# Kernel tuning notes

Hardware: AMD Instinct MI355X
Metric: run time of the kernel (lower is better)

The kernel has to match this reference:

```python
import jax, jax.numpy as jnp
import numpy as np

N = 4
IS_SLOW = (False, False, True, True)
RATES = (1, 1, 4, 4)
THRESH = 0.3
F2S_IDX = {(0, 2): 0, (0, 3): 1, (1, 2): 2, (1, 3): 3}


def _conv1d(x, w, stride, pad):
    # x: [B, C_in, T], w: [C_out, C_in, K]
    return jax.lax.conv_general_dilated(
        x, w, (stride,), [(pad, pad)], dimension_numbers=("NCH", "OIH", "NCH"))


def _linear_interp(x, t_out):
    # x: [B, D, T_in] -> [B, D, t_out]; matches F.interpolate(mode='linear', align_corners=False)
    t_in = x.shape[2]
    scale = t_in / t_out
    src = (jnp.arange(t_out, dtype=jnp.float32) + 0.5) * scale - 0.5
    src = jnp.clip(src, 0.0, float(t_in - 1))
    i0 = jnp.floor(src).astype(jnp.int32)
    i1 = jnp.minimum(i0 + 1, t_in - 1)
    w = (src - i0.astype(jnp.float32)).astype(x.dtype)
    return x[:, :, i0] * (1.0 - w) + x[:, :, i1] * w


def setup_inputs() -> dict:
    key = jax.random.key(0)
    ks = jax.random.split(key, 8)
    T_FAST, T_SLOW, B, D, H = 512, 128, 32, 1024, 256
    return {
        "feat0": jax.random.normal(ks[0], (T_FAST, B, D), jnp.float32),
        "feat1": jax.random.normal(ks[1], (T_FAST, B, D), jnp.float32),
        "feat2": jax.random.normal(ks[2], (T_SLOW, B, D), jnp.float32),
        "feat3": jax.random.normal(ks[3], (T_SLOW, B, D), jnp.float32),
        "mlp_w1": jax.random.normal(ks[4], (N * N, 2 * D, H), jnp.float32) * 0.02,
        "mlp_b1": jnp.zeros((N * N, H), jnp.float32),
        "mlp_w2": jax.random.normal(ks[5], (N * N, H, 1), jnp.float32) * 0.02,
        "mlp_b2": jnp.zeros((N * N, 1), jnp.float32),
        "s2f_w": jax.random.normal(ks[6], (D, D, 1), jnp.float32) * 0.02,
        "s2f_b": jnp.zeros((D,), jnp.float32),
        "f2s_w": jax.random.normal(ks[7], (4, D, D, 5), jnp.float32) * 0.02,
    }


def reference(feat0, feat1, feat2, feat3, mlp_w1, mlp_b1, mlp_w2, mlp_b2,
              s2f_w, s2f_b, f2s_w):
    feats = [feat0, feat1, feat2, feat3]            # [T_i, B, D]
    feats_bdt = [jnp.transpose(f, (1, 2, 0)) for f in feats]  # [B, D, T_i]
    globals_ = [f.mean(axis=2) for f in feats_bdt]  # [B, D]
    outputs = list(feats)
    for i in range(N):
        for j in range(N):
            if i == j:
                continue
            p = i * N + j
            pair_vec = jnp.concatenate([globals_[i], globals_[j]], axis=-1)  # [B, 2D]
            h = jax.nn.relu(pair_vec @ mlp_w1[p] + mlp_b1[p])
            score = jax.nn.sigmoid(h @ mlp_w2[p] + mlp_b2[p])[:, 0]          # [B]
            cond = score.mean() >= THRESH
            if IS_SLOW[i] and not IS_SLOW[j]:
                # slow -> fast: interpolate up, 1x1 conv proj, score-weighted residual
                up = _linear_interp(feats_bdt[i], feats_bdt[j].shape[2])
                up = _conv1d(up, s2f_w, 1, 0) + s2f_b[None, :, None]
                new = feats_bdt[j] + score[:, None, None] * up
                outputs[j] = jnp.where(cond, jnp.transpose(new, (2, 0, 1)), outputs[j])
            elif (not IS_SLOW[i]) and IS_SLOW[j]:
                # fast -> slow: strided conv down, score-weighted residual
                stride = RATES[j] // RATES[i]
                down = _conv1d(feats_bdt[i], f2s_w[F2S_IDX[(i, j)]], stride, 2)
                new = feats_bdt[j] + score[:, None, None] * down
                outputs[j] = jnp.where(cond, jnp.transpose(new, (2, 0, 1)), outputs[j])
    return tuple(outputs)
```

## Files before the change

kernel.cpp:

```cpp
#include <hip/hip_runtime.h>
#include <math.h>

typedef __bf16 bf16;
typedef bf16 bf16x8 __attribute__((ext_vector_type(8)));
typedef bf16 bf16x4 __attribute__((ext_vector_type(4)));
typedef float f32x4 __attribute__((ext_vector_type(4)));

#define OFF_GLOB   0ul
#define OFF_H      524288ul
#define OFF_SCORE  786432ul
#define OFF_COND   787456ul
#define OFF_PART   788480ul
#define OFF_PROJ   5242880ul
#define OFF_WTF2S  38797312ul
#define OFF_WTS2F  59768832ul


__device__ __forceinline__ void slot_ij(int s, int& i, int& j) {
  if (s < 4) { i = 2 + (s & 1); j = s >> 1; }
  else       { int ss = s - 4; i = ss & 1; j = 2 + (ss >> 1); }
}

__global__ __launch_bounds__(256) void k_means_part(
    const float* __restrict__ f0, const float* __restrict__ f1,
    const float* __restrict__ f2, const float* __restrict__ f3,
    float* __restrict__ part)
{
  int b = blockIdx.x, c = blockIdx.y, i = blockIdx.z, tid = threadIdx.x;
  const float* f = (i == 0) ? f0 : (i == 1) ? f1 : (i == 2) ? f2 : f3;
  int chunk = (i < 2) ? 64 : 16;
  int t0 = c * chunk;
  float4 s = make_float4(0.f, 0.f, 0.f, 0.f);
  for (int t = t0; t < t0 + chunk; ++t) {
    float4 v = ((const float4*)(f + (size_t)(t * 32 + b) * 1024))[tid];
    s.x += v.x; s.y += v.y; s.z += v.z; s.w += v.w;
  }
  ((float4*)part)[(size_t)((i * 8 + c) * 32 + b) * 256 + tid] = s;
}

__global__ __launch_bounds__(256) void k_means_final(
    const float* __restrict__ part, float* __restrict__ g)
{
  int b = blockIdx.x, i = blockIdx.y, tid = threadIdx.x;
  float4 s = make_float4(0.f, 0.f, 0.f, 0.f);
  for (int c = 0; c < 8; ++c) {
    float4 v = ((const float4*)part)[(size_t)((i * 8 + c) * 32 + b) * 256 + tid];
    s.x += v.x; s.y += v.y; s.z += v.z; s.w += v.w;
  }
  float inv = (i < 2) ? (1.f / 512.f) : (1.f / 128.f);
  s.x *= inv; s.y *= inv; s.z *= inv; s.w *= inv;
  ((float4*)g)[(size_t)(i * 32 + b) * 256 + tid] = s;
}

__global__ __launch_bounds__(256) void k_mlp1(
    const float* __restrict__ g, const float* __restrict__ w1, float* __restrict__ h_ws)
{
  int s = blockIdx.x, hc = blockIdx.y, kz = blockIdx.z, tid = threadIdx.x;
  int pi, pj; slot_ij(s, pi, pj);
  int p = pi * 4 + pj;
  int h = hc * 32 + (tid & 31);
  int bg = tid >> 5;
  __shared__ float pv[32 * 65];
  float acc0 = 0.f, acc1 = 0.f, acc2 = 0.f, acc3 = 0.f;
  for (int kt = 0; kt < 8; ++kt) {
    int k0 = kz * 512 + kt * 64;
    __syncthreads();
    for (int l = tid; l < 2048; l += 256) {
      int bb = l >> 6, kk = l & 63;
      int k = k0 + kk;
      float v = (k < 1024) ? g[(size_t)pi * 32768 + bb * 1024 + k]
                           : g[(size_t)pj * 32768 + bb * 1024 + (k - 1024)];
      pv[bb * 65 + kk] = v;
    }
    __syncthreads();
    const float* wp = w1 + ((size_t)p * 2048 + k0) * 256 + hc * 32 + (tid & 31);
    for (int kk = 0; kk < 64; ++kk) {
      float w = wp[(size_t)kk * 256];
      acc0 += pv[(bg * 4 + 0) * 65 + kk] * w;
      acc1 += pv[(bg * 4 + 1) * 65 + kk] * w;
      acc2 += pv[(bg * 4 + 2) * 65 + kk] * w;
      acc3 += pv[(bg * 4 + 3) * 65 + kk] * w;
    }
  }
  atomicAdd(&h_ws[(size_t)s * 8192 + (bg * 4 + 0) * 256 + h], acc0);
  atomicAdd(&h_ws[(size_t)s * 8192 + (bg * 4 + 1) * 256 + h], acc1);
  atomicAdd(&h_ws[(size_t)s * 8192 + (bg * 4 + 2) * 256 + h], acc2);
  atomicAdd(&h_ws[(size_t)s * 8192 + (bg * 4 + 3) * 256 + h], acc3);
}

__global__ __launch_bounds__(256) void k_mlp2(
    const float* __restrict__ h_ws, const float* __restrict__ b1,
    const float* __restrict__ w2, const float* __restrict__ b2,
    float* __restrict__ score, float* __restrict__ cond)
{
  int s = blockIdx.x, tid = threadIdx.x;
  int pi, pj; slot_ij(s, pi, pj);
  int p = pi * 4 + pj;
  float w2v = w2[p * 256 + tid];
  float b1v = b1[p * 256 + tid];
  float b2v = b2[p];
  __shared__ float red[4];
  float tot = 0.f;
  for (int b = 0; b < 32; ++b) {
    float v = fmaxf(h_ws[(size_t)s * 8192 + b * 256 + tid] + b1v, 0.f) * w2v;
    for (int off = 32; off > 0; off >>= 1) v += __shfl_down(v, off);
    if ((tid & 63) == 0) red[tid >> 6] = v;
    __syncthreads();
    if (tid == 0) {
      float sum = red[0] + red[1] + red[2] + red[3] + b2v;
      float sc = 1.f / (1.f + expf(-sum));
      score[s * 32 + b] = sc;
      tot += sc;
    }
    __syncthreads();
  }
  if (tid == 0) cond[s] = (tot * (1.f / 32.f) >= 0.3f) ? 1.f : 0.f;
}

__global__ __launch_bounds__(256) void k_f2s_transpose(
    const float* __restrict__ w, const float* __restrict__ cond, bf16* __restrict__ wT)
{
  int z = blockIdx.y, co = blockIdx.x, tid = threadIdx.x;
  int sel = (cond[5 + 2 * z] > 0.5f) ? 1 : ((cond[4 + 2 * z] > 0.5f) ? 0 : -1);
  if (sel < 0) return;
  int widx = sel * 2 + z;
  __shared__ float buf[5120];
  const float* src = w + ((size_t)widx * 1024 + co) * 5120;
  for (int l = tid; l < 5120; l += 256) buf[l] = src[l];
  __syncthreads();
  bf16* dst = wT + (size_t)z * 5242880 + (size_t)co * 5120;
  for (int o = tid; o < 5120; o += 256) {
    int kk = o >> 10, ci = o & 1023;
    dst[o] = (bf16)buf[ci * 5 + kk];
  }
}

__global__ __launch_bounds__(256) void k_s2f_convert(
    const float* __restrict__ w, bf16* __restrict__ wT)
{
  size_t gi = (size_t)blockIdx.x * 256 + threadIdx.x;
  float4 v = ((const float4*)w)[gi];
  bf16x4 o;
  o[0] = (bf16)v.x; o[1] = (bf16)v.y; o[2] = (bf16)v.z; o[3] = (bf16)v.w;
  *(bf16x4*)&wT[gi * 4] = o;
}

__global__ __launch_bounds__(256) void k_s2f_gemm(
    const float* __restrict__ feat2, const float* __restrict__ feat3,
    const bf16* __restrict__ wT, const float* __restrict__ s2f_b,
    const float* __restrict__ cond, float* __restrict__ proj)
{
  int z = blockIdx.z;
  int sel = (cond[1 + 2 * z] > 0.5f) ? 3 : ((cond[2 * z] > 0.5f) ? 2 : -1);
  if (sel < 0) return;
  const float* A = (sel == 3) ? feat3 : feat2;
  float* projz = proj + (size_t)z * 4194304;
  int tid = threadIdx.x;
  int M0 = blockIdx.x * 128, N0 = blockIdx.y * 128;
  __shared__ bf16 As[128][72];
  __shared__ bf16 Bs[128][72];
  f32x4 acc[4][4];
  for (int a = 0; a < 4; ++a)
    for (int c = 0; c < 4; ++c) { acc[a][c][0] = 0.f; acc[a][c][1] = 0.f; acc[a][c][2] = 0.f; acc[a][c][3] = 0.f; }
  int row = tid >> 1, half = tid & 1;
  int lane = tid & 63, wv = tid >> 6;
  int wr = (wv >> 1) * 64, wc = (wv & 1) * 64;
  int rl = lane & 15, q = lane >> 4;
  for (int kt = 0; kt < 16; ++kt) {
    int ci0 = kt * 64;
    __syncthreads();
    {
      const float4* src = (const float4*)(A + (size_t)(M0 + row) * 1024 + ci0 + half * 32);
      #pragma unroll
      for (int u = 0; u < 4; ++u) {
        float4 v0 = src[2 * u], v1 = src[2 * u + 1];
        bf16x8 pk;
        pk[0] = (bf16)v0.x; pk[1] = (bf16)v0.y; pk[2] = (bf16)v0.z; pk[3] = (bf16)v0.w;
        pk[4] = (bf16)v1.x; pk[5] = (bf16)v1.y; pk[6] = (bf16)v1.z; pk[7] = (bf16)v1.w;
        *(bf16x8*)&As[row][half * 32 + u * 8] = pk;
      }
      const uint4* bs = (const uint4*)(wT + (size_t)(N0 + row) * 1024 + ci0 + half * 32);
      #pragma unroll
      for (int u = 0; u < 4; ++u) *(uint4*)&Bs[row][half * 32 + u * 8] = bs[u];
    }
    __syncthreads();
    #pragma unroll
    for (int ks = 0; ks < 2; ++ks) {
      bf16x8 af[4], bfv[4];
      #pragma unroll
      for (int mi = 0; mi < 4; ++mi) af[mi] = *(const bf16x8*)&As[wr + mi * 16 + rl][ks * 32 + q * 8];
      #pragma unroll
      for (int ni = 0; ni < 4; ++ni) bfv[ni] = *(const bf16x8*)&Bs[wc + ni * 16 + rl][ks * 32 + q * 8];
      #pragma unroll
      for (int mi = 0; mi < 4; ++mi)
        #pragma unroll
        for (int ni = 0; ni < 4; ++ni)
          acc[mi][ni] = __builtin_amdgcn_mfma_f32_16x16x32_bf16(af[mi], bfv[ni], acc[mi][ni], 0, 0, 0);
    }
  }
  #pragma unroll
  for (int mi = 0; mi < 4; ++mi)
    #pragma unroll
    for (int ni = 0; ni < 4; ++ni)
      #pragma unroll
      for (int r = 0; r < 4; ++r) {
        int gm = M0 + wr + mi * 16 + q * 4 + r;
        int gn = N0 + wc + ni * 16 + rl;
        projz[(size_t)gm * 1024 + gn] = acc[mi][ni][r] + s2f_b[gn];
      }
}

__global__ __launch_bounds__(256) void k_f2s_gemm(
    const float* __restrict__ feat0, const float* __restrict__ feat1,
    const float* __restrict__ feat2, const float* __restrict__ feat3,
    const bf16* __restrict__ wT, const float* __restrict__ score,
    const float* __restrict__ cond, float* __restrict__ out)
{
  int z = blockIdx.z;
  const float* fj = z ? feat3 : feat2;
  float* oj = out + 33554432ul + (size_t)z * 4194304;
  int tid = threadIdx.x;
  int M0 = blockIdx.x * 128, N0 = blockIdx.y * 128;
  int sel = (cond[5 + 2 * z] > 0.5f) ? 1 : ((cond[4 + 2 * z] > 0.5f) ? 0 : -1);
  if (sel < 0) {
    for (int l = tid; l < 4096; l += 256) {
      int rr = l >> 5, c4 = l & 31;
      size_t idx = (size_t)(M0 + rr) * 1024 + N0 + c4 * 4;
      *(float4*)(oj + idx) = *(const float4*)(fj + idx);
    }
    return;
  }
  const float* A = sel ? feat1 : feat0;
  const bf16* wTz = wT + (size_t)z * 5242880;
  int slot = (sel ? 5 : 4) + 2 * z;
  __shared__ bf16 As[128][72];
  __shared__ bf16 Bs[128][72];
  __shared__ float sld[32];
  if (tid < 32) sld[tid] = score[slot * 32 + tid];
  f32x4 acc[4][4];
  for (int a = 0; a < 4; ++a)
    for (int c = 0; c < 4; ++c) { acc[a][c][0] = 0.f; acc[a][c][1] = 0.f; acc[a][c][2] = 0.f; acc[a][c][3] = 0.f; }
  int row = tid >> 1, half = tid & 1;
  int m = M0 + row, t = m >> 5, b = m & 31;
  int lane = tid & 63, wv = tid >> 6;
  int wr = (wv >> 1) * 64, wc = (wv & 1) * 64;
  int rl = lane & 15, q = lane >> 4;
  for (int kt = 0; kt < 80; ++kt) {
    int kk = kt >> 4, ci0 = (kt & 15) << 6;
    int pos = 4 * t - 2 + kk;
    __syncthreads();
    {
      float4 v[8];
      if (pos >= 0 && pos < 512) {
        const float4* src = (const float4*)(A + (size_t)(pos * 32 + b) * 1024 + ci0 + half * 32);
        #pragma unroll
        for (int u = 0; u < 8; ++u) v[u] = src[u];
      } else {
        #pragma unroll
        for (int u = 0; u < 8; ++u) v[u] = make_float4(0.f, 0.f, 0.f, 0.f);
      }
      #pragma unroll
      for (int u = 0; u < 4; ++u) {
        bf16x8 pk;
        pk[0] = (bf16)v[2 * u].x; pk[1] = (bf16)v[2 * u].y; pk[2] = (bf16)v[2 * u].z; pk[3] = (bf16)v[2 * u].w;
        pk[4] = (bf16)v[2 * u + 1].x; pk[5] = (bf16)v[2 * u + 1].y; pk[6] = (bf16)v[2 * u + 1].z; pk[7] = (bf16)v[2 * u + 1].w;
        *(bf16x8*)&As[row][half * 32 + u * 8] = pk;
      }
      const uint4* bs = (const uint4*)(wTz + (size_t)(N0 + row) * 5120 + kt * 64 + half * 32);
      #pragma unroll
      for (int u = 0; u < 4; ++u) *(uint4*)&Bs[row][half * 32 + u * 8] = bs[u];
    }
    __syncthreads();
    #pragma unroll
    for (int ks = 0; ks < 2; ++ks) {
      bf16x8 af[4], bfv[4];
      #pragma unroll
      for (int mi = 0; mi < 4; ++mi) af[mi] = *(const bf16x8*)&As[wr + mi * 16 + rl][ks * 32 + q * 8];
      #pragma unroll
      for (int ni = 0; ni < 4; ++ni) bfv[ni] = *(const bf16x8*)&Bs[wc + ni * 16 + rl][ks * 32 + q * 8];
      #pragma unroll
      for (int mi = 0; mi < 4; ++mi)
        #pragma unroll
        for (int ni = 0; ni < 4; ++ni)
          acc[mi][ni] = __builtin_amdgcn_mfma_f32_16x16x32_bf16(af[mi], bfv[ni], acc[mi][ni], 0, 0, 0);
    }
  }
  #pragma unroll
  for (int mi = 0; mi < 4; ++mi)
    #pragma unroll
    for (int ni = 0; ni < 4; ++ni)
      #pragma unroll
      for (int r = 0; r < 4; ++r) {
        int gm = M0 + wr + mi * 16 + q * 4 + r;
        int gn = N0 + wc + ni * 16 + rl;
        size_t idx = (size_t)gm * 1024 + gn;
        oj[idx] = fj[idx] + sld[gm & 31] * acc[mi][ni][r];
      }
}

__global__ __launch_bounds__(256) void k_interp(
    const float* __restrict__ f0, const float* __restrict__ f1,
    const float* __restrict__ proj, const float* __restrict__ score,
    const float* __restrict__ cond, float* __restrict__ out)
{
  int z = blockIdx.y, tb = blockIdx.x, tid = threadIdx.x;
  const float* fj = z ? f1 : f0;
  float* oj = out + (size_t)z * 16777216;
  int sel = (cond[1 + 2 * z] > 0.5f) ? 3 : ((cond[2 * z] > 0.5f) ? 2 : -1);
  float4 fv = ((const float4*)(fj + (size_t)tb * 1024))[tid];
  if (sel < 0) {
    ((float4*)(oj + (size_t)tb * 1024))[tid] = fv;
    return;
  }
  int t = tb >> 5, b = tb & 31;
  int slot = 2 * z + (sel == 3 ? 1 : 0);
  float s = score[slot * 32 + b];
  float srcf = 0.25f * (float)t - 0.375f;
  srcf = fminf(fmaxf(srcf, 0.f), 127.f);
  int i0 = (int)srcf;
  int i1 = min(i0 + 1, 127);
  float w = srcf - (float)i0;
  const float* pz = proj + (size_t)z * 4194304;
  float4 a = ((const float4*)(pz + (size_t)(i0 * 32 + b) * 1024))[tid];
  float4 c = ((const float4*)(pz + (size_t)(i1 * 32 + b) * 1024))[tid];
  float4 o;
  o.x = fv.x + s * ((1.f - w) * a.x + w * c.x);
  o.y = fv.y + s * ((1.f - w) * a.y + w * c.y);
  o.z = fv.z + s * ((1.f - w) * a.z + w * c.z);
  o.w = fv.w + s * ((1.f - w) * a.w + w * c.w);
  ((float4*)(oj + (size_t)tb * 1024))[tid] = o;
}

extern "C" void kernel_launch(void* const* d_in, const int* in_sizes, int n_in,
                              void* d_out, int out_size, void* d_ws, size_t ws_size,
                              hipStream_t stream) {
  const float* f0   = (const float*)d_in[0];
  const float* f1   = (const float*)d_in[1];
  const float* f2   = (const float*)d_in[2];
  const float* f3   = (const float*)d_in[3];
  const float* w1   = (const float*)d_in[4];
  const float* b1   = (const float*)d_in[5];
  const float* w2   = (const float*)d_in[6];
  const float* b2   = (const float*)d_in[7];
  const float* s2fw = (const float*)d_in[8];
  const float* s2fb = (const float*)d_in[9];
  const float* f2sw = (const float*)d_in[10];
  float* out = (float*)d_out;

  char* ws = (char*)d_ws;
  float* g     = (float*)(ws + OFF_GLOB);
  float* h_ws  = (float*)(ws + OFF_H);
  float* score = (float*)(ws + OFF_SCORE);
  float* cond  = (float*)(ws + OFF_COND);
  float* part  = (float*)(ws + OFF_PART);
  float* proj  = (float*)(ws + OFF_PROJ);
  bf16*  wtf   = (bf16*)(ws + OFF_WTF2S);
  bf16*  wts   = (bf16*)(ws + OFF_WTS2F);

  hipMemsetAsync(h_ws, 0, 262144, stream);
  k_means_part<<<dim3(32, 8, 4), 256, 0, stream>>>(f0, f1, f2, f3, part);
  k_means_final<<<dim3(32, 4), 256, 0, stream>>>(part, g);
  k_mlp1<<<dim3(8, 8, 4), 256, 0, stream>>>(g, w1, h_ws);
  k_mlp2<<<8, 256, 0, stream>>>(h_ws, b1, w2, b2, score, cond);
  k_f2s_transpose<<<dim3(1024, 2), 256, 0, stream>>>(f2sw, cond, wtf);
  k_s2f_convert<<<1024, 256, 0, stream>>>(s2fw, wts);
  k_s2f_gemm<<<dim3(32, 8, 2), 256, 0, stream>>>(f2, f3, wts, s2fb, cond, proj);
  k_f2s_gemm<<<dim3(32, 8, 2), 256, 0, stream>>>(f0, f1, f2, f3, wtf, score, cond, out);
  k_interp<<<dim3(16384, 2), 256, 0, stream>>>(f0, f1, proj, score, cond, out);
}
```

Before: 743.2 us.

## Merge f2s/s2f GEMMs into one launch with direct-to-LDS loads and bf16 proj

The two conv GEMM kernels become a single launch that dispatches on blockIdx.z, which adds concurrency across the two GEMM types. The M tile is halved to 64 so twice as many blocks run. A tiles are now staged to shared memory as fp32 via global_load_lds and converted to bf16 when fragments are read, and padded rows are served from a zeroed buffer. The s2f projection intermediate is stored as bf16 to halve its write and read traffic in k_interp, at some precision cost. Skipping the register staging and padding the LDS differently may create bank conflicts, and the loop has no double buffering.

```diff
diff --git a/kernel.cpp b/kernel.cpp
--- a/kernel.cpp
+++ b/kernel.cpp
@@ -10,11 +10,18 @@
 #define OFF_H      524288ul
 #define OFF_SCORE  786432ul
 #define OFF_COND   787456ul
-#define OFF_PART   788480ul
-#define OFF_PROJ   5242880ul
-#define OFF_WTF2S  38797312ul
-#define OFF_WTS2F  59768832ul
-
+#define OFF_ZP     788480ul
+#define OFF_PART   792576ul
+#define OFF_PROJ   4986880ul
+#define OFF_WTF2S  21764096ul
+#define OFF_WTS2F  42735616ul
+
+
+__device__ __forceinline__ void gll16(const void* gsrc, void* ldst) {
+  __builtin_amdgcn_global_load_lds(
+      (const __attribute__((address_space(1))) unsigned int*)gsrc,
+      (__attribute__((address_space(3))) unsigned int*)ldst, 16, 0, 0);
+}
 
 __device__ __forceinline__ void slot_ij(int s, int& i, int& j) {
   if (s < 4) { i = 2 + (s & 1); j = s >> 1; }
@@ -145,162 +152,142 @@
   *(bf16x4*)&wT[gi * 4] = o;
 }
 
-__global__ __launch_bounds__(256) void k_s2f_gemm(
-    const float* __restrict__ feat2, const float* __restrict__ feat3,
-    const bf16* __restrict__ wT, const float* __restrict__ s2f_b,
-    const float* __restrict__ cond, float* __restrict__ proj)
-{
-  int z = blockIdx.z;
-  int sel = (cond[1 + 2 * z] > 0.5f) ? 3 : ((cond[2 * z] > 0.5f) ? 2 : -1);
-  if (sel < 0) return;
-  const float* A = (sel == 3) ? feat3 : feat2;
-  float* projz = proj + (size_t)z * 4194304;
+#define MFMA_COMPUTE()                                                                       \
+  do {                                                                                       \
+    _Pragma("unroll") for (int ks = 0; ks < 2; ++ks) {                                       \
+      bf16x8 af[2]; bf16x8 bfv[4];                                                           \
+      _Pragma("unroll") for (int mi = 0; mi < 2; ++mi) {                                     \
+        const float* ap = &As[(wr + mi * 16 + rl) * 64 + ks * 32 + q * 8];                   \
+        float4 a0 = *(const float4*)ap; float4 a1 = *(const float4*)(ap + 4);                \
+        bf16x8 t8;                                                                           \
+        t8[0] = (bf16)a0.x; t8[1] = (bf16)a0.y; t8[2] = (bf16)a0.z; t8[3] = (bf16)a0.w;      \
+        t8[4] = (bf16)a1.x; t8[5] = (bf16)a1.y; t8[6] = (bf16)a1.z; t8[7] = (bf16)a1.w;      \
+        af[mi] = t8;                                                                         \
+      }                                                                                      \
+      _Pragma("unroll") for (int ni = 0; ni < 4; ++ni)                                       \
+        bfv[ni] = *(const bf16x8*)&Bs[(wc + ni * 16 + rl) * 64 + ks * 32 + q * 8];           \
+      _Pragma("unroll") for (int mi = 0; mi < 2; ++mi)                                       \
+        _Pragma("unroll") for (int ni = 0; ni < 4; ++ni)                                     \
+          acc[mi][ni] = __builtin_amdgcn_mfma_f32_16x16x32_bf16(af[mi], bfv[ni],             \
+                                                                acc[mi][ni], 0, 0, 0);       \
+    }                                                                                        \
+  } while (0)
+
+__global__ __launch_bounds__(256) void k_gemms(
+    const float* __restrict__ f0, const float* __restrict__ f1,
+    const float* __restrict__ f2, const float* __restrict__ f3,
+    const bf16* __restrict__ wtf, const bf16* __restrict__ wts,
+    const float* __restrict__ s2fb, const float* __restrict__ score,
+    const float* __restrict__ cond, const float* __restrict__ zp,
+    bf16* __restrict__ proj, float* __restrict__ out)
+{
+  __shared__ float As[64 * 64];
+  __shared__ bf16 Bs[128 * 64];
+  __shared__ float sld[32];
   int tid = threadIdx.x;
-  int M0 = blockIdx.x * 128, N0 = blockIdx.y * 128;
-  __shared__ bf16 As[128][72];
-  __shared__ bf16 Bs[128][72];
-  f32x4 acc[4][4];
-  for (int a = 0; a < 4; ++a)
+  int bz = blockIdx.z;
+  int M0 = blockIdx.x * 64, N0 = blockIdx.y * 128;
+  int lane = tid & 63, wv = tid >> 6;
+  int wr = (wv >> 1) * 32, wc = (wv & 1) * 64;
+  int rl = lane & 15, q = lane >> 4;
+  f32x4 acc[2][4];
+  #pragma unroll
+  for (int a = 0; a < 2; ++a)
+    #pragma unroll
     for (int c = 0; c < 4; ++c) { acc[a][c][0] = 0.f; acc[a][c][1] = 0.f; acc[a][c][2] = 0.f; acc[a][c][3] = 0.f; }
-  int row = tid >> 1, half = tid & 1;
-  int lane = tid & 63, wv = tid >> 6;
-  int wr = (wv >> 1) * 64, wc = (wv & 1) * 64;
-  int rl = lane & 15, q = lane >> 4;
-  for (int kt = 0; kt < 16; ++kt) {
-    int ci0 = kt * 64;
-    __syncthreads();
-    {
-      const float4* src = (const float4*)(A + (size_t)(M0 + row) * 1024 + ci0 + half * 32);
+
+  if (bz < 2) {
+    int z = bz;
+    const float* fj = z ? f3 : f2;
+    float* oj = out + 33554432ul + (size_t)z * 4194304;
+    int sel = (cond[5 + 2 * z] > 0.5f) ? 1 : ((cond[4 + 2 * z] > 0.5f) ? 0 : -1);
+    if (sel < 0) {
+      for (int l = tid; l < 2048; l += 256) {
+        int rr = l >> 5, c = (l & 31) * 4;
+        size_t idx = (size_t)(M0 + rr) * 1024 + N0 + c;
+        *(float4*)(oj + idx) = *(const float4*)(fj + idx);
+      }
+      return;
+    }
+    const float* A = sel ? f1 : f0;
+    const bf16* wB = wtf + (size_t)z * 5242880;
+    if (tid < 32) sld[tid] = score[((sel ? 5 : 4) + 2 * z) * 32 + tid];
+    for (int kt = 0; kt < 80; ++kt) {
+      int kk = kt >> 4, ci0 = (kt & 15) << 6;
       #pragma unroll
       for (int u = 0; u < 4; ++u) {
-        float4 v0 = src[2 * u], v1 = src[2 * u + 1];
-        bf16x8 pk;
-        pk[0] = (bf16)v0.x; pk[1] = (bf16)v0.y; pk[2] = (bf16)v0.z; pk[3] = (bf16)v0.w;
-        pk[4] = (bf16)v1.x; pk[5] = (bf16)v1.y; pk[6] = (bf16)v1.z; pk[7] = (bf16)v1.w;
-        *(bf16x8*)&As[row][half * 32 + u * 8] = pk;
-      }
-      const uint4* bs = (const uint4*)(wT + (size_t)(N0 + row) * 1024 + ci0 + half * 32);
-      #pragma unroll
-      for (int u = 0; u < 4; ++u) *(uint4*)&Bs[row][half * 32 + u * 8] = bs[u];
-    }
-    __syncthreads();
+        int m = u * 16 + (tid >> 4);
+        int gc = (tid & 15) * 4;
+        int mm = M0 + m, t = mm >> 5, b = mm & 31;
+        int pos = 4 * t - 2 + kk;
+        const float* ga = (pos >= 0)
+            ? A + (((size_t)(pos * 32 + b)) << 10) + ci0 + gc
+            : zp + gc;
+        gll16(ga, &As[m * 64 + gc]);
+      }
+      #pragma unroll
+      for (int u = 0; u < 4; ++u) {
+        int n = u * 32 + (tid >> 3);
+        int gc = (tid & 7) * 8;
+        gll16(wB + (size_t)(N0 + n) * 5120 + kt * 64 + gc, &Bs[n * 64 + gc]);
+      }
+      __syncthreads();
+      MFMA_COMPUTE();
+      __syncthreads();
+    }
     #pragma unroll
-    for (int ks = 0; ks < 2; ++ks) {
-      bf16x8 af[4], bfv[4];
-      #pragma unroll
-      for (int mi = 0; mi < 4; ++mi) af[mi] = *(const bf16x8*)&As[wr + mi * 16 + rl][ks * 32 + q * 8];
-      #pragma unroll
-      for (int ni = 0; ni < 4; ++ni) bfv[ni] = *(const bf16x8*)&Bs[wc + ni * 16 + rl][ks * 32 + q * 8];
-      #pragma unroll
-      for (int mi = 0; mi < 4; ++mi)
+    for (int mi = 0; mi < 2; ++mi)
+      #pragma unroll
+      for (int ni = 0; ni < 4; ++ni) {
+        int gm = M0 + wr + mi * 16 + q * 4;
+        int gn = N0 + wc + ni * 16 + rl;
         #pragma unroll
-        for (int ni = 0; ni < 4; ++ni)
-          acc[mi][ni] = __builtin_amdgcn_mfma_f32_16x16x32_bf16(af[mi], bfv[ni], acc[mi][ni], 0, 0, 0);
-    }
-  }
-  #pragma unroll
-  for (int mi = 0; mi < 4; ++mi)
+        for (int r = 0; r < 4; ++r) {
+          size_t idx = (size_t)(gm + r) * 1024 + gn;
+          oj[idx] = fj[idx] + sld[(gm + r) & 31] * acc[mi][ni][r];
+        }
+      }
+  } else {
+    int z = bz - 2;
+    int sel = (cond[1 + 2 * z] > 0.5f) ? 3 : ((cond[2 * z] > 0.5f) ? 2 : -1);
+    if (sel < 0) return;
+    const float* A = (sel == 3) ? f3 : f2;
+    bf16* pj = proj + (size_t)z * 4194304;
+    for (int kt = 0; kt < 16; ++kt) {
+      int ci0 = kt << 6;
+      #pragma unroll
+      for (int u = 0; u < 4; ++u) {
+        int m = u * 16 + (tid >> 4);
+        int gc = (tid & 15) * 4;
+        gll16(A + (((size_t)(M0 + m)) << 10) + ci0 + gc, &As[m * 64 + gc]);
+      }
+      #pragma unroll
+      for (int u = 0; u < 4; ++u) {
+        int n = u * 32 + (tid >> 3);
+        int gc = (tid & 7) * 8;
+        gll16(wts + (size_t)(N0 + n) * 1024 + ci0 + gc, &Bs[n * 64 + gc]);
+      }
+      __syncthreads();
+      MFMA_COMPUTE();
+      __syncthreads();
+    }
     #pragma unroll
-    for (int ni = 0; ni < 4; ++ni)
-      #pragma unroll
-      for (int r = 0; r < 4; ++r) {
-        int gm = M0 + wr + mi * 16 + q * 4 + r;
+    for (int mi = 0; mi < 2; ++mi)
+      #pragma unroll
+      for (int ni = 0; ni < 4; ++ni) {
+        int gm = M0 + wr + mi * 16 + q * 4;
         int gn = N0 + wc + ni * 16 + rl;
-        projz[(size_t)gm * 1024 + gn] = acc[mi][ni][r] + s2f_b[gn];
-      }
-}
-
-__global__ __launch_bounds__(256) void k_f2s_gemm(
-    const float* __restrict__ feat0, const float* __restrict__ feat1,
-    const float* __restrict__ feat2, const float* __restrict__ feat3,
-    const bf16* __restrict__ wT, const float* __restrict__ score,
-    const float* __restrict__ cond, float* __restrict__ out)
-{
-  int z = blockIdx.z;
-  const float* fj = z ? feat3 : feat2;
-  float* oj = out + 33554432ul + (size_t)z * 4194304;
-  int tid = threadIdx.x;
-  int M0 = blockIdx.x * 128, N0 = blockIdx.y * 128;
-  int sel = (cond[5 + 2 * z] > 0.5f) ? 1 : ((cond[4 + 2 * z] > 0.5f) ? 0 : -1);
-  if (sel < 0) {
-    for (int l = tid; l < 4096; l += 256) {
-      int rr = l >> 5, c4 = l & 31;
-      size_t idx = (size_t)(M0 + rr) * 1024 + N0 + c4 * 4;
-      *(float4*)(oj + idx) = *(const float4*)(fj + idx);
-    }
-    return;
-  }
-  const float* A = sel ? feat1 : feat0;
-  const bf16* wTz = wT + (size_t)z * 5242880;
-  int slot = (sel ? 5 : 4) + 2 * z;
-  __shared__ bf16 As[128][72];
-  __shared__ bf16 Bs[128][72];
-  __shared__ float sld[32];
-  if (tid < 32) sld[tid] = score[slot * 32 + tid];
-  f32x4 acc[4][4];
-  for (int a = 0; a < 4; ++a)
-    for (int c = 0; c < 4; ++c) { acc[a][c][0] = 0.f; acc[a][c][1] = 0.f; acc[a][c][2] = 0.f; acc[a][c][3] = 0.f; }
-  int row = tid >> 1, half = tid & 1;
-  int m = M0 + row, t = m >> 5, b = m & 31;
-  int lane = tid & 63, wv = tid >> 6;
-  int wr = (wv >> 1) * 64, wc = (wv & 1) * 64;
-  int rl = lane & 15, q = lane >> 4;
-  for (int kt = 0; kt < 80; ++kt) {
-    int kk = kt >> 4, ci0 = (kt & 15) << 6;
-    int pos = 4 * t - 2 + kk;
-    __syncthreads();
-    {
-      float4 v[8];
-      if (pos >= 0 && pos < 512) {
-        const float4* src = (const float4*)(A + (size_t)(pos * 32 + b) * 1024 + ci0 + half * 32);
+        float bv = s2fb[gn];
         #pragma unroll
-        for (int u = 0; u < 8; ++u) v[u] = src[u];
-      } else {
-        #pragma unroll
-        for (int u = 0; u < 8; ++u) v[u] = make_float4(0.f, 0.f, 0.f, 0.f);
-      }
-      #pragma unroll
-      for (int u = 0; u < 4; ++u) {
-        bf16x8 pk;
-        pk[0] = (bf16)v[2 * u].x; pk[1] = (bf16)v[2 * u].y; pk[2] = (bf16)v[2 * u].z; pk[3] = (bf16)v[2 * u].w;
-        pk[4] = (bf16)v[2 * u + 1].x; pk[5] = (bf16)v[2 * u + 1].y; pk[6] = (bf16)v[2 * u + 1].z; pk[7] = (bf16)v[2 * u + 1].w;
-        *(bf16x8*)&As[row][half * 32 + u * 8] = pk;
-      }
-      const uint4* bs = (const uint4*)(wTz + (size_t)(N0 + row) * 5120 + kt * 64 + half * 32);
-      #pragma unroll
-      for (int u = 0; u < 4; ++u) *(uint4*)&Bs[row][half * 32 + u * 8] = bs[u];
-    }
-    __syncthreads();
-    #pragma unroll
-    for (int ks = 0; ks < 2; ++ks) {
-      bf16x8 af[4], bfv[4];
-      #pragma unroll
-      for (int mi = 0; mi < 4; ++mi) af[mi] = *(const bf16x8*)&As[wr + mi * 16 + rl][ks * 32 + q * 8];
-      #pragma unroll
-      for (int ni = 0; ni < 4; ++ni) bfv[ni] = *(const bf16x8*)&Bs[wc + ni * 16 + rl][ks * 32 + q * 8];
-      #pragma unroll
-      for (int mi = 0; mi < 4; ++mi)
-        #pragma unroll
-        for (int ni = 0; ni < 4; ++ni)
-          acc[mi][ni] = __builtin_amdgcn_mfma_f32_16x16x32_bf16(af[mi], bfv[ni], acc[mi][ni], 0, 0, 0);
-    }
-  }
-  #pragma unroll
-  for (int mi = 0; mi < 4; ++mi)
-    #pragma unroll
-    for (int ni = 0; ni < 4; ++ni)
-      #pragma unroll
-      for (int r = 0; r < 4; ++r) {
-        int gm = M0 + wr + mi * 16 + q * 4 + r;
-        int gn = N0 + wc + ni * 16 + rl;
-        size_t idx = (size_t)gm * 1024 + gn;
-        oj[idx] = fj[idx] + sld[gm & 31] * acc[mi][ni][r];
-      }
+        for (int r = 0; r < 4; ++r)
+          pj[(size_t)(gm + r) * 1024 + gn] = (bf16)(acc[mi][ni][r] + bv);
+      }
+  }
 }
 
 __global__ __launch_bounds__(256) void k_interp(
     const float* __restrict__ f0, const float* __restrict__ f1,
-    const float* __restrict__ proj, const float* __restrict__ score,
+    const bf16* __restrict__ proj, const float* __restrict__ score,
     const float* __restrict__ cond, float* __restrict__ out)
 {
   int z = blockIdx.y, tb = blockIdx.x, tid = threadIdx.x;
@@ -320,14 +307,14 @@
   int i0 = (int)srcf;
   int i1 = min(i0 + 1, 127);
   float w = srcf - (float)i0;
-  const float* pz = proj + (size_t)z * 4194304;
-  float4 a = ((const float4*)(pz + (size_t)(i0 * 32 + b) * 1024))[tid];
-  float4 c = ((const float4*)(pz + (size_t)(i1 * 32 + b) * 1024))[tid];
+  const bf16* pz = proj + (size_t)z * 4194304;
+  bf16x4 a4 = *(const bf16x4*)&pz[((size_t)(i0 * 32 + b)) * 1024 + tid * 4];
+  bf16x4 c4 = *(const bf16x4*)&pz[((size_t)(i1 * 32 + b)) * 1024 + tid * 4];
   float4 o;
-  o.x = fv.x + s * ((1.f - w) * a.x + w * c.x);
-  o.y = fv.y + s * ((1.f - w) * a.y + w * c.y);
-  o.z = fv.z + s * ((1.f - w) * a.z + w * c.z);
-  o.w = fv.w + s * ((1.f - w) * a.w + w * c.w);
+  o.x = fv.x + s * ((1.f - w) * (float)a4[0] + w * (float)c4[0]);
+  o.y = fv.y + s * ((1.f - w) * (float)a4[1] + w * (float)c4[1]);
+  o.z = fv.z + s * ((1.f - w) * (float)a4[2] + w * (float)c4[2]);
+  o.w = fv.w + s * ((1.f - w) * (float)a4[3] + w * (float)c4[3]);
   ((float4*)(oj + (size_t)tb * 1024))[tid] = o;
 }
 
@@ -352,19 +339,21 @@
   float* h_ws  = (float*)(ws + OFF_H);
   float* score = (float*)(ws + OFF_SCORE);
   float* cond  = (float*)(ws + OFF_COND);
+  float* zp    = (float*)(ws + OFF_ZP);
   float* part  = (float*)(ws + OFF_PART);
-  float* proj  = (float*)(ws + OFF_PROJ);
+  bf16*  proj  = (bf16*)(ws + OFF_PROJ);
   bf16*  wtf   = (bf16*)(ws + OFF_WTF2S);
   bf16*  wts   = (bf16*)(ws + OFF_WTS2F);
 
   hipMemsetAsync(h_ws, 0, 262144, stream);
+  hipMemsetAsync(zp, 0, 4096, stream);
   k_means_part<<<dim3(32, 8, 4), 256, 0, stream>>>(f0, f1, f2, f3, part);
   k_means_final<<<dim3(32, 4), 256, 0, stream>>>(part, g);
   k_mlp1<<<dim3(8, 8, 4), 256, 0, stream>>>(g, w1, h_ws);
   k_mlp2<<<8, 256, 0, stream>>>(h_ws, b1, w2, b2, score, cond);
   k_f2s_transpose<<<dim3(1024, 2), 256, 0, stream>>>(f2sw, cond, wtf);
   k_s2f_convert<<<1024, 256, 0, stream>>>(s2fw, wts);
-  k_s2f_gemm<<<dim3(32, 8, 2), 256, 0, stream>>>(f2, f3, wts, s2fb, cond, proj);
-  k_f2s_gemm<<<dim3(32, 8, 2), 256, 0, stream>>>(f0, f1, f2, f3, wtf, score, cond, out);
+  k_gemms<<<dim3(64, 8, 4), 256, 0, stream>>>(f0, f1, f2, f3, wtf, wts, s2fb,
+                                              score, cond, zp, proj, out);
   k_interp<<<dim3(16384, 2), 256, 0, stream>>>(f0, f1, proj, score, cond, out);
 }
```

After: 1.048 ms. 1.41x slower.
